# Kernel optimization log

Hardware: AMD Instinct MI355X
Metric: run time of the kernel (lower is better)

## Reference

```python
import jax, jax.numpy as jnp
import numpy as np

B, M, GRID = 4, 8192, 32          # batches, points per batch, voxel grid side
N = B * M
K = 8                              # knn neighbors (includes self at dist 0)
C_IN, C_OUT, H = 8, 8, 128
KEYB = 64                          # hash base (coords shifted +1 stay in [0,33])
EPS = 1e-5


def setup_inputs() -> dict:
    rng = np.random.default_rng(0)
    # unique occupied voxels per batch (ME SparseTensor requires unique coords)
    cs = []
    for b in range(B):
        lin = rng.choice(GRID ** 3, size=M, replace=False)
        x, y, z = lin // (GRID * GRID), (lin // GRID) % GRID, lin % GRID
        cs.append(np.stack([np.full(M, b), x, y, z], axis=1))
    coords = jnp.asarray(np.concatenate(cs, axis=0).astype(np.int32))  # [N,4]

    key = jax.random.key(0)
    ks = jax.random.split(key, 4)
    feats = jax.random.normal(ks[0], (N, C_IN), jnp.float32)
    w1 = jax.random.normal(ks[1], ((K + 1) * C_IN, H), jnp.float32) * 0.05  # 1x1 conv
    g1 = jnp.ones((H,), jnp.float32)
    b1 = jnp.zeros((H,), jnp.float32)
    w3 = jax.random.normal(ks[2], (27, H, H), jnp.float32) * 0.02          # 3^3 sparse conv
    g2 = jnp.ones((H,), jnp.float32)
    b2 = jnp.zeros((H,), jnp.float32)
    w_out = jax.random.normal(ks[3], (H, 2 * C_OUT), jnp.float32) * 0.05   # 1x1 conv
    return dict(coords=coords, feats=feats, w1=w1, g1=g1, b1=b1,
                w3=w3, g2=g2, b2=b2, w_out=w_out)


def _knn_idx(coords):
    # per-batch brute-force kNN on xyz (batch column segments the search)
    xyz = coords[:, 1:].astype(jnp.float32).reshape(B, M, 3)
    d2 = jnp.sum((xyz[:, :, None, :] - xyz[:, None, :, :]) ** 2, -1)  # [B,M,M]
    _, idx = jax.lax.top_k(-d2, K)                                     # [B,M,K]
    return (idx + (jnp.arange(B) * M)[:, None, None]).reshape(N, K)


def _bn(x, g, b):
    mu = jnp.mean(x, axis=0)
    var = jnp.var(x, axis=0)
    return (x - mu) * jax.lax.rsqrt(var + EPS) * g + b


def reference(coords, feats, w1, g1, b1, w3, g2, b2, w_out):
    # --- kNN gather-and-build: [center || k neighbor feats] -> (k+1)*C_in ---
    nbr = _knn_idx(coords)                                        # [N,K] int
    combined = jnp.concatenate([feats[:, None, :], feats[nbr]], axis=1)
    combined = combined.reshape(N, (K + 1) * C_IN)
    # --- neighbor_processor: 1x1 conv + BN + ReLU ---
    h = jax.nn.relu(_bn(combined @ w1, g1, b1))                   # [N,H]
    # --- context_predictor conv k=3: gather inputs at coord+offset via hash ---
    c = coords[:, 1:] + 1                                         # shift so offsets stay >= 0
    keys = ((coords[:, 0] * KEYB + c[:, 0]) * KEYB + c[:, 1]) * KEYB + c[:, 2]
    order = jnp.argsort(keys)
    skeys = keys[order]
    offs = jnp.stack(jnp.meshgrid(*([jnp.arange(-1, 2)] * 3), indexing='ij'),
                     axis=-1).reshape(27, 3)                      # {-1,0,1}^3
    okey = (offs[:, 0] * KEYB + offs[:, 1]) * KEYB + offs[:, 2]   # [27]
    q = keys[None, :] + okey[:, None]                             # [27,N]
    pos = jnp.clip(jnp.searchsorted(skeys, q), 0, N - 1)
    valid = skeys[pos] == q                                       # [27,N]
    j = order[pos]                                                # [27,N]
    gathered = jnp.where(valid[..., None], h[j], 0.0)             # [27,N,H]
    h2 = jnp.einsum('onc,ocd->nd', gathered, w3)                  # [N,H]
    h2 = jax.nn.relu(_bn(h2, g2, b2))
    # --- final 1x1 conv -> mean/scale ---
    return h2 @ w_out                                             # [N, 2*C_OUT]
```

## Files before the change

### kernel.cpp

```cpp
#include <hip/hip_runtime.h>
#include <hip/hip_bf16.h>

#define B_   4
#define M_   8192
#define N_   32768
#define H_   128
#define EPS_ 1e-5f
#define TBL  1048576
#define GUARD 8192

typedef short short8 __attribute__((ext_vector_type(8)));
typedef float f32x4  __attribute__((ext_vector_type(4)));

__global__ __launch_bounds__(256) void prep_pack_kernel(const int* __restrict__ coords,
                                                        int* __restrict__ table,
                                                        int* __restrict__ packed,
                                                        int* __restrict__ keyb,
                                                        const float* __restrict__ w3,
                                                        ushort* __restrict__ w3f,
                                                        float* __restrict__ gsum1,
                                                        float* __restrict__ gsum2,
                                                        int* __restrict__ flagcnt,
                                                        unsigned int* __restrict__ hbz) {
    int bid = blockIdx.x, tid = threadIdx.x;
    if (bid < 128) {
        int n = bid * 256 + tid;
        int b = coords[4*n+0], x = coords[4*n+1], y = coords[4*n+2], z = coords[4*n+3];
        packed[n] = (x << 10) | (y << 5) | z;
        int key = ((b*64 + x+1)*64 + y+1)*64 + (z+1);
        keyb[n] = key;
        table[key] = n;
        if (bid < 8)  gsum1[bid*256 + tid] = 0.f;
        if (bid == 0) gsum2[tid] = 0.f;
        if (bid == 8 && tid < 64) hbz[tid] = 0u;
        if (bid == 9 && tid == 0) *flagcnt = 0;
        return;
    }
    int t = (bid - 128) * 256 + tid;
    int lane = t & 63;
    int ct   = (t >> 6) & 7;
    int ks   = (t >> 9) & 3;
    int o    = t >> 11;
    int quad = lane >> 4, l15 = lane & 15;
    int n = ct*16 + l15;
    const float* src = w3 + o*16384;
    ushort out8[8];
#pragma unroll
    for (int j = 0; j < 8; ++j) {
        int c = ks*32 + quad*8 + j;
        float v = src[c*128 + n];
        __hip_bfloat16 bv = __float2bfloat16(v);
        ushort u; __builtin_memcpy(&u, &bv, 2);
        out8[j] = u;
    }
    *(uint4*)&w3f[t*8] = *(uint4*)out8;
}

__global__ __launch_bounds__(256) void knn_window_kernel(const int* __restrict__ table,
                                                         const int* __restrict__ keyb,
                                                         int* __restrict__ nbr,
                                                         int* __restrict__ flagcnt,
                                                         int* __restrict__ flaglist) {
    __shared__ int okey_sh[93], d2_sh[93];
    __shared__ int tops[256 * 8];
    __shared__ int ncnt;
    int tid = threadIdx.x;
    if (tid == 0) ncnt = 0;
    __syncthreads();
    if (tid < 125) {
        int dx = tid / 25 - 2, rr = tid % 25, dy = rr / 5 - 2, dz = rr % 5 - 2;
        int d2 = dx*dx + dy*dy + dz*dz;
        if (d2 <= 8) {
            int p = atomicAdd(&ncnt, 1);
            okey_sh[p] = dx * 4096 + dy * 64 + dz;
            d2_sh[p]   = d2;
        }
    }
    __syncthreads();

    int q   = blockIdx.x * 64 + (tid >> 2);
    int sub = tid & 3;
    int kb  = keyb[q];

    int top[8];
#pragma unroll
    for (int k = 0; k < 8; ++k) top[k] = 0x7FFFFFFF;

    int base = sub * 24;
    int cnt  = (sub == 3) ? 21 : 24;
    for (int i = 0; i < cnt; ++i) {
        int idx = base + i;
        int j = table[kb + okey_sh[idx]];
        if (j >= 0) {
            int key = (d2_sh[idx] << 13) | (j & 8191);
            if (key < top[7]) {
#pragma unroll
                for (int k = 7; k >= 1; --k)
                    top[k] = (key < top[k]) ? max(key, top[k-1]) : top[k];
                top[0] = min(key, top[0]);
            }
        }
    }
#pragma unroll
    for (int k = 0; k < 8; ++k) tops[tid*8 + k] = top[k];
    __syncthreads();

    if (sub == 0) {
        const int* L = &tops[tid*8];
        int ia0 = 0, ia1 = 0, ia2 = 0, ia3 = 0;
        int res[8];
#pragma unroll
        for (int k = 0; k < 8; ++k) {
            int v0 = L[ia0], v1 = L[8 + ia1], v2 = L[16 + ia2], v3 = L[24 + ia3];
            int m01 = min(v0, v1), m23 = min(v2, v3);
            int m = min(m01, m23);
            res[k] = m;
            if (m == v0) ++ia0; else if (m == v1) ++ia1;
            else if (m == v2) ++ia2; else ++ia3;
        }
        int bb = q & ~(M_-1);
        if ((res[7] >> 13) <= 8) {
#pragma unroll
            for (int k = 0; k < 8; ++k) nbr[q*8 + k] = bb + (res[k] & 8191);
        } else {
            int pos = atomicAdd(flagcnt, 1);
            flaglist[pos] = q;
        }
    }
}

__global__ __launch_bounds__(256) void knn_bf_kernel(const int* __restrict__ packed,
                                                     const int* __restrict__ flagcnt,
                                                     const int* __restrict__ flaglist,
                                                     int* __restrict__ nbr) {
    __shared__ int tops[256 * 8];
    int tid = threadIdx.x;
    int cnt = *flagcnt;
    for (int f = blockIdx.x; f < cnt; f += gridDim.x) {
        int n = flaglist[f];
        int bb = n & ~(M_-1);
        int p = packed[n];
        int qx = (p >> 10) & 31, qy = (p >> 5) & 31, qz = p & 31;
        int top[8];
#pragma unroll
        for (int k = 0; k < 8; ++k) top[k] = 0x7FFFFFFF;
        for (int j = tid; j < M_; j += 256) {
            int c = packed[bb + j];
            int dx = qx - ((c >> 10) & 31);
            int dy = qy - ((c >> 5) & 31);
            int dz = qz - (c & 31);
            int d2 = dx*dx + dy*dy + dz*dz;
            int key = (d2 << 13) | j;
            if (key < top[7]) {
#pragma unroll
                for (int k = 7; k >= 1; --k)
                    top[k] = (key < top[k]) ? max(key, top[k-1]) : top[k];
                top[0] = min(key, top[0]);
            }
        }
#pragma unroll
        for (int k = 0; k < 8; ++k) tops[tid*8 + k] = top[k];
        __syncthreads();
        for (int stride = 128; stride >= 1; stride >>= 1) {
            if (tid < stride) {
                int* A  = &tops[tid*8];
                int* Bp = &tops[(tid+stride)*8];
                int r[8]; int ia = 0, ib = 0;
#pragma unroll
                for (int k = 0; k < 8; ++k) {
                    int a = A[ia], b2 = Bp[ib];
                    if (a <= b2) { r[k] = a; ++ia; } else { r[k] = b2; ++ib; }
                }
#pragma unroll
                for (int k = 0; k < 8; ++k) A[k] = r[k];
            }
            __syncthreads();
        }
        if (tid == 0) {
#pragma unroll
            for (int k = 0; k < 8; ++k) nbr[n*8 + k] = bb + (tops[k] & 8191);
        }
        __syncthreads();
    }
}

__global__ __launch_bounds__(256) void h1_kernel(const float* __restrict__ feats,
                                                 const int* __restrict__ nbr,
                                                 const float* __restrict__ w1,
                                                 float* __restrict__ hpre,
                                                 float* __restrict__ gsum1) {
    __shared__ float comb[16][72];
    __shared__ float ssum[256], ssq[256];
    int tid = threadIdx.x;
    int rowbase = blockIdx.x * 16;
    if (tid < 144) {
        int r = tid / 9, s = tid % 9;
        int grow = rowbase + r;
        int idx = (s == 0) ? grow : nbr[grow*8 + (s-1)];
        const float4* f = (const float4*)(feats + idx * 8);
        float4 a = f[0], b = f[1];
        float* dp = &comb[r][s*8];
        dp[0]=a.x; dp[1]=a.y; dp[2]=a.z; dp[3]=a.w;
        dp[4]=b.x; dp[5]=b.y; dp[6]=b.z; dp[7]=b.w;
    }
    __syncthreads();
    int c = tid & 127, rh = tid >> 7;
    float acc[8];
#pragma unroll
    for (int i = 0; i < 8; ++i) acc[i] = 0.f;
    for (int s = 0; s < 72; ++s) {
        float w = w1[s*128 + c];
#pragma unroll
        for (int i = 0; i < 8; ++i)
            acc[i] += comb[rh*8 + i][s] * w;
    }
    float s = 0.f, q = 0.f;
#pragma unroll
    for (int i = 0; i < 8; ++i) {
        hpre[(rowbase + rh*8 + i)*128 + c] = acc[i];
        s += acc[i]; q += acc[i]*acc[i];
    }
    ssum[tid] = s; ssq[tid] = q;
    __syncthreads();
    if (tid < 128) {
        float S = ssum[tid] + ssum[tid+128];
        float Q = ssq[tid]  + ssq[tid+128];
        float* g = gsum1 + (blockIdx.x & 7) * 256;
        atomicAdd(&g[tid], S);
        atomicAdd(&g[128 + tid], Q);
    }
}

__global__ __launch_bounds__(256) void bnrelu_bf16_kernel(const float* __restrict__ x,
                                                          const float* __restrict__ gsum1,
                                                          const float* __restrict__ g1,
                                                          const float* __restrict__ b1,
                                                          ushort* __restrict__ y) {
    __shared__ float sc[128], sh[128];
    int tid = threadIdx.x;
    if (tid < 128) {
        float s = 0.f, q = 0.f;
#pragma unroll
        for (int r = 0; r < 8; ++r) {
            s += gsum1[r*256 + tid];
            q += gsum1[r*256 + 128 + tid];
        }
        float mu  = s / (float)N_;
        float var = q / (float)N_ - mu*mu;
        float inv = rsqrtf(var + EPS_);
        float scv = inv * g1[tid];
        sc[tid] = scv;
        sh[tid] = b1[tid] - mu * scv;
    }
    __syncthreads();
    int i = blockIdx.x * 256 + tid;
    float4 v = ((const float4*)x)[i];
    int c = (i * 4) & 127;
    v.x = fmaxf(0.f, v.x*sc[c]   + sh[c]);
    v.y = fmaxf(0.f, v.y*sc[c+1] + sh[c+1]);
    v.z = fmaxf(0.f, v.z*sc[c+2] + sh[c+2]);
    v.w = fmaxf(0.f, v.w*sc[c+3] + sh[c+3]);
    ushort o[4];
#pragma unroll
    for (int k = 0; k < 4; ++k) {
        float f = (&v.x)[k];
        __hip_bfloat16 bv = __float2bfloat16(f);
        __builtin_memcpy(&o[k], &bv, 2);
    }
    ((ushort4*)y)[i] = make_ushort4(o[0], o[1], o[2], o[3]);
}

#define CONV3_LDS 145408
__global__ __launch_bounds__(512) void conv3_mfma_kernel(const ushort* __restrict__ hb,
                                                         const ushort* __restrict__ w3f,
                                                         const int* __restrict__ table,
                                                         const int* __restrict__ keyb,
                                                         float* __restrict__ h2,
                                                         float* __restrict__ gsum) {
    extern __shared__ char smem_raw[];
    ushort* Asb = (ushort*)smem_raw;
    ushort* Bsb = (ushort*)(smem_raw + 65536);
    int*    jsh = (int*)(smem_raw + 131072);
    int*    kbsh= (int*)(smem_raw + 144896);

    int tid = threadIdx.x;
    int lane = tid & 63, wid = tid >> 6;
    int quad = lane >> 4, l15 = lane & 15;
    int bid = blockIdx.x;
    int swz = (bid & 7) * 32 + (bid >> 3);
    int rowbase = swz * 128;
    int wr = wid >> 1;
    int cb = (wid & 1) * 4;

    if (tid < 128) kbsh[tid] = keyb[rowbase + tid];
    __syncthreads();
    for (int t = tid; t < 27*128; t += 512) {
        int o = t >> 7, r = t & 127;
        int dx = o/9 - 1, dy = (o/3)%3 - 1, dz = o%3 - 1;
        jsh[t] = table[kbsh[r] + dx*4096 + dy*64 + dz];
    }
    __syncthreads();

#pragma unroll
    for (int i = 0; i < 4; ++i) {
        int flat = i*512 + tid;
        int r = flat >> 4, cp = flat & 15;
        int j = jsh[r];
        const ushort* asrc = hb + j*128 + ((cp ^ (r & 15)) << 3);
        __builtin_amdgcn_global_load_lds(
            (const __attribute__((address_space(1))) unsigned int*)asrc,
            (__attribute__((address_space(3))) unsigned int*)&Asb[flat << 3],
            16, 0, 0);
        __builtin_amdgcn_global_load_lds(
            (const __attribute__((address_space(1))) unsigned int*)(w3f + (flat << 3)),
            (__attribute__((address_space(3))) unsigned int*)&Bsb[flat << 3],
            16, 0, 0);
    }
    __syncthreads();

    f32x4 acc[2][4];
#pragma unroll
    for (int i = 0; i < 2; ++i)
#pragma unroll
        for (int c = 0; c < 4; ++c)
            acc[i][c] = (f32x4){0.f, 0.f, 0.f, 0.f};

    int cur = 0;
#pragma unroll 1
    for (int o = 0; o < 27; ++o) {
        if (o < 26) {
            int obase = (o + 1) << 7;
            const ushort* wsrc = w3f + ((o + 1) << 14);
            int dst = (cur ^ 1) * 16384;
#pragma unroll
            for (int i = 0; i < 4; ++i) {
                int flat = i*512 + tid;
                int r = flat >> 4, cp = flat & 15;
                int j = jsh[obase + r];
                const ushort* asrc = hb + j*128 + ((cp ^ (r & 15)) << 3);
                __builtin_amdgcn_global_load_lds(
                    (const __attribute__((address_space(1))) unsigned int*)asrc,
                    (__attribute__((address_space(3))) unsigned int*)&Asb[dst + (flat << 3)],
                    16, 0, 0);
                __builtin_amdgcn_global_load_lds(
                    (const __attribute__((address_space(1))) unsigned int*)(wsrc + (flat << 3)),
                    (__attribute__((address_space(3))) unsigned int*)&Bsb[dst + (flat << 3)],
                    16, 0, 0);
            }
        }
        const ushort* Ac = Asb + cur*16384;
        const ushort* Bc = Bsb + cur*16384;
#pragma unroll
        for (int ks = 0; ks < 4; ++ks) {
            short8 af[2], bfr[4];
#pragma unroll
            for (int i = 0; i < 2; ++i) {
                int lr = wr*32 + i*16 + l15;
                int chunk = (ks*4 + quad) ^ l15;
                af[i] = *(const short8*)&Ac[lr*128 + chunk*8];
            }
#pragma unroll
            for (int c = 0; c < 4; ++c)
                bfr[c] = *(const short8*)&Bc[((ks*8 + cb + c)*64 + lane) << 3];
#pragma unroll
            for (int i = 0; i < 2; ++i)
#pragma unroll
                for (int c = 0; c < 4; ++c)
                    acc[i][c] = __builtin_amdgcn_mfma_f32_16x16x32_bf16(af[i], bfr[c], acc[i][c], 0, 0, 0);
        }
        __syncthreads();
        cur ^= 1;
    }

    float s[4], q[4];
#pragma unroll
    for (int c = 0; c < 4; ++c) { s[c] = 0.f; q[c] = 0.f; }
#pragma unroll
    for (int i = 0; i < 2; ++i)
#pragma unroll
        for (int c = 0; c < 4; ++c)
#pragma unroll
            for (int r = 0; r < 4; ++r) {
                int row = rowbase + wr*32 + i*16 + quad*4 + r;
                int col = (cb + c)*16 + l15;
                float v = acc[i][c][r];
                h2[row*128 + col] = v;
                s[c] += v; q[c] += v*v;
            }
    float* red = (float*)smem_raw;
    if (tid < 256) red[tid] = 0.f;
    __syncthreads();
#pragma unroll
    for (int c = 0; c < 4; ++c) {
        int col = (cb + c)*16 + l15;
        atomicAdd(&red[col], s[c]);
        atomicAdd(&red[128 + col], q[c]);
    }
    __syncthreads();
    if (tid < 256) atomicAdd(&gsum[tid], red[tid]);
}

__global__ __launch_bounds__(256) void out_kernel(const float* __restrict__ h2,
                                                  const float* __restrict__ wout,
                                                  const float* __restrict__ gsum2,
                                                  const float* __restrict__ g2,
                                                  const float* __restrict__ b2,
                                                  float* __restrict__ out) {
    __shared__ float hrow[128][129];
    __shared__ float wsh[2048];
    __shared__ float sc[128], sh[128];
    int tid = threadIdx.x;
    if (tid < 128) {
        float s = gsum2[tid], q = gsum2[128 + tid];
        float mu  = s / (float)N_;
        float var = q / (float)N_ - mu*mu;
        float inv = rsqrtf(var + EPS_);
        float scv = inv * g2[tid];
        sc[tid] = scv;
        sh[tid] = b2[tid] - mu * scv;
    }
#pragma unroll
    for (int i = 0; i < 8; ++i) wsh[i*256 + tid] = wout[i*256 + tid];
    __syncthreads();

    int rowbase = blockIdx.x * 128;
#pragma unroll
    for (int i = 0; i < 16; ++i) {
        int flat = i*256 + tid;
        int row = flat >> 5, c4 = (flat & 31) * 4;
        float4 v = *(const float4*)&h2[(rowbase + row)*128 + c4];
        float4 scv = *(const float4*)&sc[c4];
        float4 shv = *(const float4*)&sh[c4];
        hrow[row][c4+0] = fmaxf(0.f, fmaf(v.x, scv.x, shv.x));
        hrow[row][c4+1] = fmaxf(0.f, fmaf(v.y, scv.y, shv.y));
        hrow[row][c4+2] = fmaxf(0.f, fmaf(v.z, scv.z, shv.z));
        hrow[row][c4+3] = fmaxf(0.f, fmaf(v.w, scv.w, shv.w));
    }
    __syncthreads();

    int row = tid >> 1, dbase = (tid & 1) * 8;
    float acc[8];
#pragma unroll
    for (int k = 0; k < 8; ++k) acc[k] = 0.f;
    for (int c = 0; c < 128; ++c) {
        float hv = hrow[row][c];
        float4 w0 = *(const float4*)&wsh[c*16 + dbase];
        float4 w1 = *(const float4*)&wsh[c*16 + dbase + 4];
        acc[0] = fmaf(hv, w0.x, acc[0]);
        acc[1] = fmaf(hv, w0.y, acc[1]);
        acc[2] = fmaf(hv, w0.z, acc[2]);
        acc[3] = fmaf(hv, w0.w, acc[3]);
        acc[4] = fmaf(hv, w1.x, acc[4]);
        acc[5] = fmaf(hv, w1.y, acc[5]);
        acc[6] = fmaf(hv, w1.z, acc[6]);
        acc[7] = fmaf(hv, w1.w, acc[7]);
    }
    float* op = out + (rowbase + row)*16 + dbase;
    *(float4*)op       = (float4){acc[0], acc[1], acc[2], acc[3]};
    *(float4*)(op + 4) = (float4){acc[4], acc[5], acc[6], acc[7]};
}

extern "C" void kernel_launch(void* const* d_in, const int* in_sizes, int n_in,
                              void* d_out, int out_size, void* d_ws, size_t ws_size,
                              hipStream_t stream) {
    const int*   coords = (const int*)d_in[0];
    const float* feats  = (const float*)d_in[1];
    const float* w1     = (const float*)d_in[2];
    const float* g1     = (const float*)d_in[3];
    const float* b1     = (const float*)d_in[4];
    const float* w3     = (const float*)d_in[5];
    const float* g2     = (const float*)d_in[6];
    const float* b2     = (const float*)d_in[7];
    const float* wout   = (const float*)d_in[8];
    float* out = (float*)d_out;

    char* ws = (char*)d_ws;
    int*    table_base = (int*)(ws);
    int*    table   = table_base + GUARD;
    int*    packed  = (int*)(ws + (4352u<<10));
    int*    keyb    = (int*)(ws + (4608u<<10));
    int*    nbr     = (int*)(ws + (4864u<<10));
    int*    flagcnt = (int*)(ws + (5888u<<10));
    int*    flaglist= (int*)(ws + (5892u<<10));
    float*  gsum2   = (float*)(ws + (6416u<<10));
    float*  gsum1   = (float*)(ws + (6420u<<10));
    ushort* w3f     = (ushort*)(ws + (6656u<<10));
    ushort* hb      = (ushort*)(ws + (7680u<<10));
    float*  h       = (float*)(ws + (15872u<<10));
    float*  h2      = h;

    static bool conv3_attr_set = false;
    if (!conv3_attr_set) {
        hipFuncSetAttribute(reinterpret_cast<const void*>(&conv3_mfma_kernel),
                            hipFuncAttributeMaxDynamicSharedMemorySize, CONV3_LDS);
        conv3_attr_set = true;
    }

    hipMemsetAsync(table_base, 0xFF, (TBL + GUARD) * sizeof(int), stream);
    prep_pack_kernel <<<344, 256, 0, stream>>>(coords, table, packed, keyb, w3, w3f,
                                               gsum1, gsum2, flagcnt,
                                               (unsigned int*)(hb - 128));
    knn_window_kernel<<<N_/64, 256, 0, stream>>>(table, keyb, nbr, flagcnt, flaglist);
    knn_bf_kernel    <<<256, 256, 0, stream>>>(packed, flagcnt, flaglist, nbr);
    h1_kernel        <<<N_/16, 256, 0, stream>>>(feats, nbr, w1, h, gsum1);
    bnrelu_bf16_kernel<<<(N_*H_/4)/256, 256, 0, stream>>>(h, gsum1, g1, b1, hb);
    conv3_mfma_kernel<<<N_/128, 512, CONV3_LDS, stream>>>(hb, w3f, table, keyb, h2, gsum2);
    out_kernel       <<<N_/128, 256, 0, stream>>>(h2, wout, gsum2, g2, b2, out);
}
```

Before: 194.3 us.

## Fuse all pipeline stages into one cooperative persistent kernel with grid syncs

Replaces the memset and seven separate kernel launches with a single cooperative kernel of 256 blocks x 512 threads that runs every stage (table init, packing, kNN window and brute force, h1, BN/ReLU, MFMA conv, output) and separates them with grid.sync(). The aim is to remove launch overhead and inter-kernel gaps. In exchange, each stage runs at one block per CU with a fixed grid, so occupancy drops for stages that used many small blocks before. Grid-wide barriers also cost time, and the table memset now runs as a strided store loop.

Result: slower. 535.0 us (+175.3%).

```diff
diff --git a/kernel.cpp b/kernel.cpp
--- a/kernel.cpp
+++ b/kernel.cpp
@@ -1,5 +1,8 @@
 #include <hip/hip_runtime.h>
+#include <hip/hip_cooperative_groups.h>
 #include <hip/hip_bf16.h>
+
+namespace cg = cooperative_groups;
 
 #define B_   4
 #define M_   8192
@@ -8,456 +11,430 @@
 #define EPS_ 1e-5f
 #define TBL  1048576
 #define GUARD 8192
+#define NTHREADS 131072
 
 typedef short short8 __attribute__((ext_vector_type(8)));
 typedef float f32x4  __attribute__((ext_vector_type(4)));
 
-__global__ __launch_bounds__(256) void prep_pack_kernel(const int* __restrict__ coords,
-                                                        int* __restrict__ table,
-                                                        int* __restrict__ packed,
-                                                        int* __restrict__ keyb,
-                                                        const float* __restrict__ w3,
-                                                        ushort* __restrict__ w3f,
-                                                        float* __restrict__ gsum1,
-                                                        float* __restrict__ gsum2,
-                                                        int* __restrict__ flagcnt,
-                                                        unsigned int* __restrict__ hbz) {
-    int bid = blockIdx.x, tid = threadIdx.x;
-    if (bid < 128) {
-        int n = bid * 256 + tid;
+#define MEGA_LDS 145408
+
+__device__ __forceinline__ ushort f2bf(float f) {
+    __hip_bfloat16 bv = __float2bfloat16(f);
+    ushort u; __builtin_memcpy(&u, &bv, 2);
+    return u;
+}
+
+__global__ __launch_bounds__(512, 1) void mega_kernel(
+        const int* __restrict__ coords, const float* __restrict__ feats,
+        const float* __restrict__ w1, const float* __restrict__ g1,
+        const float* __restrict__ b1, const float* __restrict__ w3,
+        const float* __restrict__ g2, const float* __restrict__ b2,
+        const float* __restrict__ wout, float* __restrict__ out,
+        int* __restrict__ table_base, int* __restrict__ packed,
+        int* __restrict__ keyb, int* __restrict__ nbr,
+        int* __restrict__ flagcnt, int* __restrict__ flaglist,
+        float* __restrict__ gsum1, float* __restrict__ gsum2,
+        ushort* __restrict__ w3f, ushort* __restrict__ hb,
+        float* __restrict__ h) {
+    extern __shared__ char smem_raw[];
+    cg::grid_group grid = cg::this_grid();
+    int tid = threadIdx.x, bid = blockIdx.x;
+    int gid = bid * 512 + tid;
+    int* table = table_base + GUARD;
+    float* h2 = h;
+
+    for (int idx = gid; idx < TBL + GUARD; idx += NTHREADS) table_base[idx] = -1;
+    if (gid < N_) {
+        int n = gid;
         int b = coords[4*n+0], x = coords[4*n+1], y = coords[4*n+2], z = coords[4*n+3];
         packed[n] = (x << 10) | (y << 5) | z;
-        int key = ((b*64 + x+1)*64 + y+1)*64 + (z+1);
-        keyb[n] = key;
-        table[key] = n;
-        if (bid < 8)  gsum1[bid*256 + tid] = 0.f;
-        if (bid == 0) gsum2[tid] = 0.f;
-        if (bid == 8 && tid < 64) hbz[tid] = 0u;
-        if (bid == 9 && tid == 0) *flagcnt = 0;
-        return;
-    }
-    int t = (bid - 128) * 256 + tid;
-    int lane = t & 63;
-    int ct   = (t >> 6) & 7;
-    int ks   = (t >> 9) & 3;
-    int o    = t >> 11;
-    int quad = lane >> 4, l15 = lane & 15;
-    int n = ct*16 + l15;
-    const float* src = w3 + o*16384;
-    ushort out8[8];
-#pragma unroll
-    for (int j = 0; j < 8; ++j) {
-        int c = ks*32 + quad*8 + j;
-        float v = src[c*128 + n];
-        __hip_bfloat16 bv = __float2bfloat16(v);
-        ushort u; __builtin_memcpy(&u, &bv, 2);
-        out8[j] = u;
-    }
-    *(uint4*)&w3f[t*8] = *(uint4*)out8;
-}
-
-__global__ __launch_bounds__(256) void knn_window_kernel(const int* __restrict__ table,
-                                                         const int* __restrict__ keyb,
-                                                         int* __restrict__ nbr,
-                                                         int* __restrict__ flagcnt,
-                                                         int* __restrict__ flaglist) {
-    __shared__ int okey_sh[93], d2_sh[93];
-    __shared__ int tops[256 * 8];
-    __shared__ int ncnt;
-    int tid = threadIdx.x;
-    if (tid == 0) ncnt = 0;
-    __syncthreads();
-    if (tid < 125) {
-        int dx = tid / 25 - 2, rr = tid % 25, dy = rr / 5 - 2, dz = rr % 5 - 2;
-        int d2 = dx*dx + dy*dy + dz*dz;
-        if (d2 <= 8) {
-            int p = atomicAdd(&ncnt, 1);
-            okey_sh[p] = dx * 4096 + dy * 64 + dz;
-            d2_sh[p]   = d2;
-        }
-    }
-    __syncthreads();
-
-    int q   = blockIdx.x * 64 + (tid >> 2);
-    int sub = tid & 3;
-    int kb  = keyb[q];
-
-    int top[8];
-#pragma unroll
-    for (int k = 0; k < 8; ++k) top[k] = 0x7FFFFFFF;
-
-    int base = sub * 24;
-    int cnt  = (sub == 3) ? 21 : 24;
-    for (int i = 0; i < cnt; ++i) {
-        int idx = base + i;
-        int j = table[kb + okey_sh[idx]];
-        if (j >= 0) {
-            int key = (d2_sh[idx] << 13) | (j & 8191);
-            if (key < top[7]) {
-#pragma unroll
-                for (int k = 7; k >= 1; --k)
-                    top[k] = (key < top[k]) ? max(key, top[k-1]) : top[k];
-                top[0] = min(key, top[0]);
-            }
-        }
-    }
-#pragma unroll
-    for (int k = 0; k < 8; ++k) tops[tid*8 + k] = top[k];
-    __syncthreads();
-
-    if (sub == 0) {
-        const int* L = &tops[tid*8];
-        int ia0 = 0, ia1 = 0, ia2 = 0, ia3 = 0;
-        int res[8];
-#pragma unroll
-        for (int k = 0; k < 8; ++k) {
-            int v0 = L[ia0], v1 = L[8 + ia1], v2 = L[16 + ia2], v3 = L[24 + ia3];
-            int m01 = min(v0, v1), m23 = min(v2, v3);
-            int m = min(m01, m23);
-            res[k] = m;
-            if (m == v0) ++ia0; else if (m == v1) ++ia1;
-            else if (m == v2) ++ia2; else ++ia3;
-        }
-        int bb = q & ~(M_-1);
-        if ((res[7] >> 13) <= 8) {
-#pragma unroll
-            for (int k = 0; k < 8; ++k) nbr[q*8 + k] = bb + (res[k] & 8191);
-        } else {
-            int pos = atomicAdd(flagcnt, 1);
-            flaglist[pos] = q;
-        }
-    }
-}
-
-__global__ __launch_bounds__(256) void knn_bf_kernel(const int* __restrict__ packed,
-                                                     const int* __restrict__ flagcnt,
-                                                     const int* __restrict__ flaglist,
-                                                     int* __restrict__ nbr) {
-    __shared__ int tops[256 * 8];
-    int tid = threadIdx.x;
-    int cnt = *flagcnt;
-    for (int f = blockIdx.x; f < cnt; f += gridDim.x) {
-        int n = flaglist[f];
-        int bb = n & ~(M_-1);
-        int p = packed[n];
-        int qx = (p >> 10) & 31, qy = (p >> 5) & 31, qz = p & 31;
+        keyb[n] = ((b*64 + x+1)*64 + y+1)*64 + (z+1);
+    }
+    if (gid < 55296) {
+        int t = gid;
+        int tl = t & 63;
+        int ct = (t >> 6) & 7, ks = (t >> 9) & 3, o = t >> 11;
+        int tq = tl >> 4, t15 = tl & 15;
+        int n = ct*16 + t15;
+        const float* src = w3 + o*16384;
+        ushort out8[8];
+#pragma unroll
+        for (int j = 0; j < 8; ++j)
+            out8[j] = f2bf(src[(ks*32 + tq*8 + j)*128 + n]);
+        *(uint4*)&w3f[t*8] = *(uint4*)out8;
+    }
+    if (gid < 2048) gsum1[gid] = 0.f;
+    if (gid < 256)  gsum2[gid] = 0.f;
+    if (gid < 64)   ((unsigned int*)(hb - 128))[gid] = 0u;
+    if (gid == 0)   *flagcnt = 0;
+    grid.sync();
+
+    if (gid < N_) table[keyb[gid]] = gid;
+    grid.sync();
+
+    {
+        int* okey_sh = (int*)smem_raw;
+        int* d2_sh   = (int*)(smem_raw + 512);
+        int* tops    = (int*)(smem_raw + 1024);
+        __shared__ int ncnt;
+        if (tid == 0) ncnt = 0;
+        __syncthreads();
+        if (tid < 125) {
+            int dx = tid / 25 - 2, rr = tid % 25, dy = rr / 5 - 2, dz = rr % 5 - 2;
+            int d2 = dx*dx + dy*dy + dz*dz;
+            if (d2 <= 8) {
+                int p = atomicAdd(&ncnt, 1);
+                okey_sh[p] = dx * 4096 + dy * 64 + dz;
+                d2_sh[p]   = d2;
+            }
+        }
+        __syncthreads();
+
+        int q   = bid * 128 + (tid >> 2);
+        int sub = tid & 3;
+        int kb  = keyb[q];
         int top[8];
 #pragma unroll
         for (int k = 0; k < 8; ++k) top[k] = 0x7FFFFFFF;
-        for (int j = tid; j < M_; j += 256) {
-            int c = packed[bb + j];
-            int dx = qx - ((c >> 10) & 31);
-            int dy = qy - ((c >> 5) & 31);
-            int dz = qz - (c & 31);
-            int d2 = dx*dx + dy*dy + dz*dz;
-            int key = (d2 << 13) | j;
-            if (key < top[7]) {
-#pragma unroll
-                for (int k = 7; k >= 1; --k)
-                    top[k] = (key < top[k]) ? max(key, top[k-1]) : top[k];
-                top[0] = min(key, top[0]);
+        int base = sub * 24;
+        int cnt  = (sub == 3) ? 21 : 24;
+        for (int i = 0; i < cnt; ++i) {
+            int idx = base + i;
+            int j = table[kb + okey_sh[idx]];
+            if (j >= 0) {
+                int key = (d2_sh[idx] << 13) | (j & 8191);
+                if (key < top[7]) {
+#pragma unroll
+                    for (int k = 7; k >= 1; --k)
+                        top[k] = (key < top[k]) ? max(key, top[k-1]) : top[k];
+                    top[0] = min(key, top[0]);
+                }
             }
         }
 #pragma unroll
         for (int k = 0; k < 8; ++k) tops[tid*8 + k] = top[k];
         __syncthreads();
-        for (int stride = 128; stride >= 1; stride >>= 1) {
-            if (tid < stride) {
-                int* A  = &tops[tid*8];
-                int* Bp = &tops[(tid+stride)*8];
-                int r[8]; int ia = 0, ib = 0;
-#pragma unroll
-                for (int k = 0; k < 8; ++k) {
-                    int a = A[ia], b2 = Bp[ib];
-                    if (a <= b2) { r[k] = a; ++ia; } else { r[k] = b2; ++ib; }
-                }
-#pragma unroll
-                for (int k = 0; k < 8; ++k) A[k] = r[k];
-            }
+
+        if (sub == 0) {
+            const int* L = &tops[tid*8];
+            int ia0 = 0, ia1 = 0, ia2 = 0, ia3 = 0;
+            int res[8];
+#pragma unroll
+            for (int k = 0; k < 8; ++k) {
+                int v0 = L[ia0], v1 = L[8 + ia1], v2 = L[16 + ia2], v3 = L[24 + ia3];
+                int m01 = min(v0, v1), m23 = min(v2, v3);
+                int m = min(m01, m23);
+                res[k] = m;
+                if (m == v0) ++ia0; else if (m == v1) ++ia1;
+                else if (m == v2) ++ia2; else ++ia3;
+            }
+            int bb = q & ~(M_-1);
+            if ((res[7] >> 13) <= 8) {
+#pragma unroll
+                for (int k = 0; k < 8; ++k) nbr[q*8 + k] = bb + (res[k] & 8191);
+            } else {
+                int pos = atomicAdd(flagcnt, 1);
+                flaglist[pos] = q;
+            }
+        }
+    }
+    grid.sync();
+
+    {
+        int* tops = (int*)smem_raw;
+        int cnt = atomicAdd(flagcnt, 0);
+        for (int f = bid; f < cnt; f += 256) {
+            int n = flaglist[f];
+            int bb = n & ~(M_-1);
+            int p = packed[n];
+            int qx = (p >> 10) & 31, qy = (p >> 5) & 31, qz = p & 31;
+            int top[8];
+#pragma unroll
+            for (int k = 0; k < 8; ++k) top[k] = 0x7FFFFFFF;
+            for (int j = tid; j < M_; j += 512) {
+                int c = packed[bb + j];
+                int dx = qx - ((c >> 10) & 31);
+                int dy = qy - ((c >> 5) & 31);
+                int dz = qz - (c & 31);
+                int d2 = dx*dx + dy*dy + dz*dz;
+                int key = (d2 << 13) | j;
+                if (key < top[7]) {
+#pragma unroll
+                    for (int k = 7; k >= 1; --k)
+                        top[k] = (key < top[k]) ? max(key, top[k-1]) : top[k];
+                    top[0] = min(key, top[0]);
+                }
+            }
+#pragma unroll
+            for (int k = 0; k < 8; ++k) tops[tid*8 + k] = top[k];
             __syncthreads();
-        }
-        if (tid == 0) {
-#pragma unroll
-            for (int k = 0; k < 8; ++k) nbr[n*8 + k] = bb + (tops[k] & 8191);
-        }
-        __syncthreads();
-    }
-}
-
-__global__ __launch_bounds__(256) void h1_kernel(const float* __restrict__ feats,
-                                                 const int* __restrict__ nbr,
-                                                 const float* __restrict__ w1,
-                                                 float* __restrict__ hpre,
-                                                 float* __restrict__ gsum1) {
-    __shared__ float comb[16][72];
-    __shared__ float ssum[256], ssq[256];
-    int tid = threadIdx.x;
-    int rowbase = blockIdx.x * 16;
-    if (tid < 144) {
-        int r = tid / 9, s = tid % 9;
-        int grow = rowbase + r;
-        int idx = (s == 0) ? grow : nbr[grow*8 + (s-1)];
-        const float4* f = (const float4*)(feats + idx * 8);
-        float4 a = f[0], b = f[1];
-        float* dp = &comb[r][s*8];
-        dp[0]=a.x; dp[1]=a.y; dp[2]=a.z; dp[3]=a.w;
-        dp[4]=b.x; dp[5]=b.y; dp[6]=b.z; dp[7]=b.w;
-    }
-    __syncthreads();
-    int c = tid & 127, rh = tid >> 7;
-    float acc[8];
-#pragma unroll
-    for (int i = 0; i < 8; ++i) acc[i] = 0.f;
-    for (int s = 0; s < 72; ++s) {
-        float w = w1[s*128 + c];
-#pragma unroll
-        for (int i = 0; i < 8; ++i)
-            acc[i] += comb[rh*8 + i][s] * w;
-    }
-    float s = 0.f, q = 0.f;
-#pragma unroll
-    for (int i = 0; i < 8; ++i) {
-        hpre[(rowbase + rh*8 + i)*128 + c] = acc[i];
-        s += acc[i]; q += acc[i]*acc[i];
-    }
-    ssum[tid] = s; ssq[tid] = q;
-    __syncthreads();
-    if (tid < 128) {
-        float S = ssum[tid] + ssum[tid+128];
-        float Q = ssq[tid]  + ssq[tid+128];
-        float* g = gsum1 + (blockIdx.x & 7) * 256;
-        atomicAdd(&g[tid], S);
-        atomicAdd(&g[128 + tid], Q);
-    }
-}
-
-__global__ __launch_bounds__(256) void bnrelu_bf16_kernel(const float* __restrict__ x,
-                                                          const float* __restrict__ gsum1,
-                                                          const float* __restrict__ g1,
-                                                          const float* __restrict__ b1,
-                                                          ushort* __restrict__ y) {
-    __shared__ float sc[128], sh[128];
-    int tid = threadIdx.x;
-    if (tid < 128) {
-        float s = 0.f, q = 0.f;
-#pragma unroll
-        for (int r = 0; r < 8; ++r) {
-            s += gsum1[r*256 + tid];
-            q += gsum1[r*256 + 128 + tid];
-        }
-        float mu  = s / (float)N_;
-        float var = q / (float)N_ - mu*mu;
-        float inv = rsqrtf(var + EPS_);
-        float scv = inv * g1[tid];
-        sc[tid] = scv;
-        sh[tid] = b1[tid] - mu * scv;
-    }
-    __syncthreads();
-    int i = blockIdx.x * 256 + tid;
-    float4 v = ((const float4*)x)[i];
-    int c = (i * 4) & 127;
-    v.x = fmaxf(0.f, v.x*sc[c]   + sh[c]);
-    v.y = fmaxf(0.f, v.y*sc[c+1] + sh[c+1]);
-    v.z = fmaxf(0.f, v.z*sc[c+2] + sh[c+2]);
-    v.w = fmaxf(0.f, v.w*sc[c+3] + sh[c+3]);
-    ushort o[4];
-#pragma unroll
-    for (int k = 0; k < 4; ++k) {
-        float f = (&v.x)[k];
-        __hip_bfloat16 bv = __float2bfloat16(f);
-        __builtin_memcpy(&o[k], &bv, 2);
-    }
-    ((ushort4*)y)[i] = make_ushort4(o[0], o[1], o[2], o[3]);
-}
-
-#define CONV3_LDS 145408
-__global__ __launch_bounds__(512) void conv3_mfma_kernel(const ushort* __restrict__ hb,
-                                                         const ushort* __restrict__ w3f,
-                                                         const int* __restrict__ table,
-                                                         const int* __restrict__ keyb,
-                                                         float* __restrict__ h2,
-                                                         float* __restrict__ gsum) {
-    extern __shared__ char smem_raw[];
-    ushort* Asb = (ushort*)smem_raw;
-    ushort* Bsb = (ushort*)(smem_raw + 65536);
-    int*    jsh = (int*)(smem_raw + 131072);
-    int*    kbsh= (int*)(smem_raw + 144896);
-
-    int tid = threadIdx.x;
-    int lane = tid & 63, wid = tid >> 6;
-    int quad = lane >> 4, l15 = lane & 15;
-    int bid = blockIdx.x;
-    int swz = (bid & 7) * 32 + (bid >> 3);
-    int rowbase = swz * 128;
-    int wr = wid >> 1;
-    int cb = (wid & 1) * 4;
-
-    if (tid < 128) kbsh[tid] = keyb[rowbase + tid];
-    __syncthreads();
-    for (int t = tid; t < 27*128; t += 512) {
-        int o = t >> 7, r = t & 127;
-        int dx = o/9 - 1, dy = (o/3)%3 - 1, dz = o%3 - 1;
-        jsh[t] = table[kbsh[r] + dx*4096 + dy*64 + dz];
-    }
-    __syncthreads();
-
-#pragma unroll
-    for (int i = 0; i < 4; ++i) {
-        int flat = i*512 + tid;
-        int r = flat >> 4, cp = flat & 15;
-        int j = jsh[r];
-        const ushort* asrc = hb + j*128 + ((cp ^ (r & 15)) << 3);
-        __builtin_amdgcn_global_load_lds(
-            (const __attribute__((address_space(1))) unsigned int*)asrc,
-            (__attribute__((address_space(3))) unsigned int*)&Asb[flat << 3],
-            16, 0, 0);
-        __builtin_amdgcn_global_load_lds(
-            (const __attribute__((address_space(1))) unsigned int*)(w3f + (flat << 3)),
-            (__attribute__((address_space(3))) unsigned int*)&Bsb[flat << 3],
-            16, 0, 0);
-    }
-    __syncthreads();
-
-    f32x4 acc[2][4];
-#pragma unroll
-    for (int i = 0; i < 2; ++i)
-#pragma unroll
-        for (int c = 0; c < 4; ++c)
-            acc[i][c] = (f32x4){0.f, 0.f, 0.f, 0.f};
-
-    int cur = 0;
+            for (int stride = 256; stride >= 1; stride >>= 1) {
+                if (tid < stride) {
+                    int* A  = &tops[tid*8];
+                    int* Bp = &tops[(tid+stride)*8];
+                    int r[8]; int ia = 0, ib = 0;
+#pragma unroll
+                    for (int k = 0; k < 8; ++k) {
+                        int a = A[ia], b2v = Bp[ib];
+                        if (a <= b2v) { r[k] = a; ++ia; } else { r[k] = b2v; ++ib; }
+                    }
+#pragma unroll
+                    for (int k = 0; k < 8; ++k) A[k] = r[k];
+                }
+                __syncthreads();
+            }
+            if (tid == 0) {
+#pragma unroll
+                for (int k = 0; k < 8; ++k) nbr[n*8 + k] = bb + (tops[k] & 8191);
+            }
+            __syncthreads();
+        }
+    }
+    grid.sync();
+
+    {
+        float (*comb)[72] = (float(*)[72])smem_raw;
+        float* ssum = (float*)(smem_raw + 12288);
+        float* ssq  = (float*)(smem_raw + 14336);
+        int c = tid & 127, rh = tid >> 7;
+        float sAcc = 0.f, qAcc = 0.f;
+        for (int it = 0; it < 4; ++it) {
+            int rowbase = bid*128 + it*32;
+            __syncthreads();
+            if (tid < 288) {
+                int r = tid / 9, s = tid % 9;
+                int grow = rowbase + r;
+                int idx = (s == 0) ? grow : nbr[grow*8 + (s-1)];
+                const float4* f4 = (const float4*)(feats + idx * 8);
+                float4 a = f4[0], b4 = f4[1];
+                float* dp = &comb[r][s*8];
+                dp[0]=a.x; dp[1]=a.y; dp[2]=a.z; dp[3]=a.w;
+                dp[4]=b4.x; dp[5]=b4.y; dp[6]=b4.z; dp[7]=b4.w;
+            }
+            __syncthreads();
+            float acc[8];
+#pragma unroll
+            for (int i = 0; i < 8; ++i) acc[i] = 0.f;
+            for (int s = 0; s < 72; ++s) {
+                float w = w1[s*128 + c];
+#pragma unroll
+                for (int i = 0; i < 8; ++i)
+                    acc[i] += comb[rh*8 + i][s] * w;
+            }
+#pragma unroll
+            for (int i = 0; i < 8; ++i) {
+                h[(rowbase + rh*8 + i)*128 + c] = acc[i];
+                sAcc += acc[i]; qAcc += acc[i]*acc[i];
+            }
+        }
+        ssum[tid] = sAcc; ssq[tid] = qAcc;
+        __syncthreads();
+        if (tid < 128) {
+            float S = ssum[tid] + ssum[tid+128] + ssum[tid+256] + ssum[tid+384];
+            float Q = ssq[tid]  + ssq[tid+128]  + ssq[tid+256]  + ssq[tid+384];
+            float* g = gsum1 + (bid & 7) * 256;
+            atomicAdd(&g[tid], S);
+            atomicAdd(&g[128 + tid], Q);
+        }
+    }
+    grid.sync();
+
+    {
+        float* sc = (float*)smem_raw;
+        float* sh = (float*)(smem_raw + 512);
+        if (tid < 128) {
+            float s = 0.f, q = 0.f;
+#pragma unroll
+            for (int r = 0; r < 8; ++r) {
+                s += gsum1[r*256 + tid];
+                q += gsum1[r*256 + 128 + tid];
+            }
+            float mu  = s / (float)N_;
+            float var = q / (float)N_ - mu*mu;
+            float inv = rsqrtf(var + EPS_);
+            float scv = inv * g1[tid];
+            sc[tid] = scv;
+            sh[tid] = b1[tid] - mu * scv;
+        }
+        __syncthreads();
+        for (int i = gid; i < N_*H_/4; i += NTHREADS) {
+            float4 v = ((const float4*)h)[i];
+            int c = (i * 4) & 127;
+            v.x = fmaxf(0.f, v.x*sc[c]   + sh[c]);
+            v.y = fmaxf(0.f, v.y*sc[c+1] + sh[c+1]);
+            v.z = fmaxf(0.f, v.z*sc[c+2] + sh[c+2]);
+            v.w = fmaxf(0.f, v.w*sc[c+3] + sh[c+3]);
+            ((ushort4*)hb)[i] = make_ushort4(f2bf(v.x), f2bf(v.y), f2bf(v.z), f2bf(v.w));
+        }
+    }
+    grid.sync();
+
+    {
+        ushort* Asb = (ushort*)smem_raw;
+        ushort* Bsb = (ushort*)(smem_raw + 65536);
+        int*    jsh = (int*)(smem_raw + 131072);
+        int*    kbsh= (int*)(smem_raw + 144896);
+        int lane = tid & 63, wid = tid >> 6;
+        int quad = lane >> 4, l15 = lane & 15;
+        int swz = (bid & 7) * 32 + (bid >> 3);
+        int rowbase = swz * 128;
+        int wr = wid >> 1;
+        int cb = (wid & 1) * 4;
+
+        if (tid < 128) kbsh[tid] = keyb[rowbase + tid];
+        __syncthreads();
+        for (int t = tid; t < 27*128; t += 512) {
+            int o = t >> 7, r = t & 127;
+            int dx = o/9 - 1, dy = (o/3)%3 - 1, dz = o%3 - 1;
+            jsh[t] = table[kbsh[r] + dx*4096 + dy*64 + dz];
+        }
+        __syncthreads();
+
+#pragma unroll
+        for (int i = 0; i < 4; ++i) {
+            int flat = i*512 + tid;
+            int r = flat >> 4, cp = flat & 15;
+            int j = jsh[r];
+            const ushort* asrc = hb + j*128 + ((cp ^ (r & 15)) << 3);
+            __builtin_amdgcn_global_load_lds(
+                (const __attribute__((address_space(1))) unsigned int*)asrc,
+                (__attribute__((address_space(3))) unsigned int*)&Asb[flat << 3],
+                16, 0, 0);
+            __builtin_amdgcn_global_load_lds(
+                (const __attribute__((address_space(1))) unsigned int*)(w3f + (flat << 3)),
+                (__attribute__((address_space(3))) unsigned int*)&Bsb[flat << 3],
+                16, 0, 0);
+        }
+        __syncthreads();
+
+        f32x4 acc[2][4];
+#pragma unroll
+        for (int i = 0; i < 2; ++i)
+#pragma unroll
+            for (int c = 0; c < 4; ++c)
+                acc[i][c] = (f32x4){0.f, 0.f, 0.f, 0.f};
+
+        int cur = 0;
 #pragma unroll 1
-    for (int o = 0; o < 27; ++o) {
-        if (o < 26) {
-            int obase = (o + 1) << 7;
-            const ushort* wsrc = w3f + ((o + 1) << 14);
-            int dst = (cur ^ 1) * 16384;
-#pragma unroll
-            for (int i = 0; i < 4; ++i) {
-                int flat = i*512 + tid;
-                int r = flat >> 4, cp = flat & 15;
-                int j = jsh[obase + r];
-                const ushort* asrc = hb + j*128 + ((cp ^ (r & 15)) << 3);
-                __builtin_amdgcn_global_load_lds(
-                    (const __attribute__((address_space(1))) unsigned int*)asrc,
-                    (__attribute__((address_space(3))) unsigned int*)&Asb[dst + (flat << 3)],
-                    16, 0, 0);
-                __builtin_amdgcn_global_load_lds(
-                    (const __attribute__((address_space(1))) unsigned int*)(wsrc + (flat << 3)),
-                    (__attribute__((address_space(3))) unsigned int*)&Bsb[dst + (flat << 3)],
-                    16, 0, 0);
-            }
-        }
-        const ushort* Ac = Asb + cur*16384;
-        const ushort* Bc = Bsb + cur*16384;
-#pragma unroll
-        for (int ks = 0; ks < 4; ++ks) {
-            short8 af[2], bfr[4];
-#pragma unroll
-            for (int i = 0; i < 2; ++i) {
-                int lr = wr*32 + i*16 + l15;
-                int chunk = (ks*4 + quad) ^ l15;
-                af[i] = *(const short8*)&Ac[lr*128 + chunk*8];
-            }
+        for (int o = 0; o < 27; ++o) {
+            if (o < 26) {
+                int obase = (o + 1) << 7;
+                const ushort* wsrc = w3f + ((o + 1) << 14);
+                int dst = (cur ^ 1) * 16384;
+#pragma unroll
+                for (int i = 0; i < 4; ++i) {
+                    int flat = i*512 + tid;
+                    int r = flat >> 4, cp = flat & 15;
+                    int j = jsh[obase + r];
+                    const ushort* asrc = hb + j*128 + ((cp ^ (r & 15)) << 3);
+                    __builtin_amdgcn_global_load_lds(
+                        (const __attribute__((address_space(1))) unsigned int*)asrc,
+                        (__attribute__((address_space(3))) unsigned int*)&Asb[dst + (flat << 3)],
+                        16, 0, 0);
+                    __builtin_amdgcn_global_load_lds(
+                        (const __attribute__((address_space(1))) unsigned int*)(wsrc + (flat << 3)),
+                        (__attribute__((address_space(3))) unsigned int*)&Bsb[dst + (flat << 3)],
+                        16, 0, 0);
+                }
+            }
+            const ushort* Ac = Asb + cur*16384;
+            const ushort* Bc = Bsb + cur*16384;
+#pragma unroll
+            for (int ks = 0; ks < 4; ++ks) {
+                short8 af[2], bfr[4];
+#pragma unroll
+                for (int i = 0; i < 2; ++i) {
+                    int lr = wr*32 + i*16 + l15;
+                    int chunk = (ks*4 + quad) ^ l15;
+                    af[i] = *(const short8*)&Ac[lr*128 + chunk*8];
+                }
+#pragma unroll
+                for (int c = 0; c < 4; ++c)
+                    bfr[c] = *(const short8*)&Bc[((ks*8 + cb + c)*64 + lane) << 3];
+#pragma unroll
+                for (int i = 0; i < 2; ++i)
+#pragma unroll
+                    for (int c = 0; c < 4; ++c)
+                        acc[i][c] = __builtin_amdgcn_mfma_f32_16x16x32_bf16(af[i], bfr[c], acc[i][c], 0, 0, 0);
+            }
+            __syncthreads();
+            cur ^= 1;
+        }
+
+        float s[4], q[4];
+#pragma unroll
+        for (int c = 0; c < 4; ++c) { s[c] = 0.f; q[c] = 0.f; }
+#pragma unroll
+        for (int i = 0; i < 2; ++i)
 #pragma unroll
             for (int c = 0; c < 4; ++c)
-                bfr[c] = *(const short8*)&Bc[((ks*8 + cb + c)*64 + lane) << 3];
-#pragma unroll
-            for (int i = 0; i < 2; ++i)
-#pragma unroll
-                for (int c = 0; c < 4; ++c)
-                    acc[i][c] = __builtin_amdgcn_mfma_f32_16x16x32_bf16(af[i], bfr[c], acc[i][c], 0, 0, 0);
-        }
-        __syncthreads();
-        cur ^= 1;
-    }
-
-    float s[4], q[4];
-#pragma unroll
-    for (int c = 0; c < 4; ++c) { s[c] = 0.f; q[c] = 0.f; }
-#pragma unroll
-    for (int i = 0; i < 2; ++i)
-#pragma unroll
-        for (int c = 0; c < 4; ++c)
-#pragma unroll
-            for (int r = 0; r < 4; ++r) {
-                int row = rowbase + wr*32 + i*16 + quad*4 + r;
-                int col = (cb + c)*16 + l15;
-                float v = acc[i][c][r];
-                h2[row*128 + col] = v;
-                s[c] += v; q[c] += v*v;
-            }
-    float* red = (float*)smem_raw;
-    if (tid < 256) red[tid] = 0.f;
-    __syncthreads();
-#pragma unroll
-    for (int c = 0; c < 4; ++c) {
-        int col = (cb + c)*16 + l15;
-        atomicAdd(&red[col], s[c]);
-        atomicAdd(&red[128 + col], q[c]);
-    }
-    __syncthreads();
-    if (tid < 256) atomicAdd(&gsum[tid], red[tid]);
-}
-
-__global__ __launch_bounds__(256) void out_kernel(const float* __restrict__ h2,
-                                                  const float* __restrict__ wout,
-                                                  const float* __restrict__ gsum2,
-                                                  const float* __restrict__ g2,
-                                                  const float* __restrict__ b2,
-                                                  float* __restrict__ out) {
-    __shared__ float hrow[128][129];
-    __shared__ float wsh[2048];
-    __shared__ float sc[128], sh[128];
-    int tid = threadIdx.x;
-    if (tid < 128) {
-        float s = gsum2[tid], q = gsum2[128 + tid];
-        float mu  = s / (float)N_;
-        float var = q / (float)N_ - mu*mu;
-        float inv = rsqrtf(var + EPS_);
-        float scv = inv * g2[tid];
-        sc[tid] = scv;
-        sh[tid] = b2[tid] - mu * scv;
-    }
-#pragma unroll
-    for (int i = 0; i < 8; ++i) wsh[i*256 + tid] = wout[i*256 + tid];
-    __syncthreads();
-
-    int rowbase = blockIdx.x * 128;
-#pragma unroll
-    for (int i = 0; i < 16; ++i) {
-        int flat = i*256 + tid;
-        int row = flat >> 5, c4 = (flat & 31) * 4;
-        float4 v = *(const float4*)&h2[(rowbase + row)*128 + c4];
-        float4 scv = *(const float4*)&sc[c4];
-        float4 shv = *(const float4*)&sh[c4];
-        hrow[row][c4+0] = fmaxf(0.f, fmaf(v.x, scv.x, shv.x));
-        hrow[row][c4+1] = fmaxf(0.f, fmaf(v.y, scv.y, shv.y));
-        hrow[row][c4+2] = fmaxf(0.f, fmaf(v.z, scv.z, shv.z));
-        hrow[row][c4+3] = fmaxf(0.f, fmaf(v.w, scv.w, shv.w));
-    }
-    __syncthreads();
-
-    int row = tid >> 1, dbase = (tid & 1) * 8;
-    float acc[8];
-#pragma unroll
-    for (int k = 0; k < 8; ++k) acc[k] = 0.f;
-    for (int c = 0; c < 128; ++c) {
-        float hv = hrow[row][c];
-        float4 w0 = *(const float4*)&wsh[c*16 + dbase];
-        float4 w1 = *(const float4*)&wsh[c*16 + dbase + 4];
-        acc[0] = fmaf(hv, w0.x, acc[0]);
-        acc[1] = fmaf(hv, w0.y, acc[1]);
-        acc[2] = fmaf(hv, w0.z, acc[2]);
-        acc[3] = fmaf(hv, w0.w, acc[3]);
-        acc[4] = fmaf(hv, w1.x, acc[4]);
-        acc[5] = fmaf(hv, w1.y, acc[5]);
-        acc[6] = fmaf(hv, w1.z, acc[6]);
-        acc[7] = fmaf(hv, w1.w, acc[7]);
-    }
-    float* op = out + (rowbase + row)*16 + dbase;
-    *(float4*)op       = (float4){acc[0], acc[1], acc[2], acc[3]};
-    *(float4*)(op + 4) = (float4){acc[4], acc[5], acc[6], acc[7]};
+#pragma unroll
+                for (int r = 0; r < 4; ++r) {
+                    int row = rowbase + wr*32 + i*16 + quad*4 + r;
+                    int col = (cb + c)*16 + l15;
+                    float v = acc[i][c][r];
+                    h2[row*128 + col] = v;
+                    s[c] += v; q[c] += v*v;
+                }
+        float* red = (float*)smem_raw;
+        __syncthreads();
+        if (tid < 256) red[tid] = 0.f;
+        __syncthreads();
+#pragma unroll
+        for (int c = 0; c < 4; ++c) {
+            int col = (cb + c)*16 + l15;
+            atomicAdd(&red[col], s[c]);
+            atomicAdd(&red[128 + col], q[c]);
+        }
+        __syncthreads();
+        if (tid < 256) atomicAdd(&gsum2[tid], red[tid]);
+    }
+    grid.sync();
+
+    {
+        float (*hrow)[129] = (float(*)[129])smem_raw;
+        float* wsh = (float*)(smem_raw + 66048);
+        float* sc  = (float*)(smem_raw + 74240);
+        float* sh  = (float*)(smem_raw + 74752);
+        if (tid < 128) {
+            float s = gsum2[tid], q = gsum2[128 + tid];
+            float mu  = s / (float)N_;
+            float var = q / (float)N_ - mu*mu;
+            float inv = rsqrtf(var + EPS_);
+            float scv = inv * g2[tid];
+            sc[tid] = scv;
+            sh[tid] = b2[tid] - mu * scv;
+        }
+        for (int i = tid; i < 2048; i += 512) wsh[i] = wout[i];
+        __syncthreads();
+
+        int rowbase = bid * 128;
+#pragma unroll
+        for (int i = 0; i < 8; ++i) {
+            int flat = i*512 + tid;
+            int row = flat >> 5, c4 = (flat & 31) * 4;
+            float4 v = *(const float4*)&h2[(rowbase + row)*128 + c4];
+            float4 scv = *(const float4*)&sc[c4];
+            float4 shv = *(const float4*)&sh[c4];
+            hrow[row][c4+0] = fmaxf(0.f, fmaf(v.x, scv.x, shv.x));
+            hrow[row][c4+1] = fmaxf(0.f, fmaf(v.y, scv.y, shv.y));
+            hrow[row][c4+2] = fmaxf(0.f, fmaf(v.z, scv.z, shv.z));
+            hrow[row][c4+3] = fmaxf(0.f, fmaf(v.w, scv.w, shv.w));
+        }
+        __syncthreads();
+
+        int row = tid >> 2, dbase = (tid & 3) * 4;
+        float a0 = 0.f, a1 = 0.f, a2 = 0.f, a3 = 0.f;
+        for (int c = 0; c < 128; ++c) {
+            float hv = hrow[row][c];
+            float4 w = *(const float4*)&wsh[c*16 + dbase];
+            a0 = fmaf(hv, w.x, a0);
+            a1 = fmaf(hv, w.y, a1);
+            a2 = fmaf(hv, w.z, a2);
+            a3 = fmaf(hv, w.w, a3);
+        }
+        *(float4*)&out[(rowbase + row)*16 + dbase] = (float4){a0, a1, a2, a3};
+    }
 }
 
 extern "C" void kernel_launch(void* const* d_in, const int* in_sizes, int n_in,
@@ -476,7 +453,6 @@
 
     char* ws = (char*)d_ws;
     int*    table_base = (int*)(ws);
-    int*    table   = table_base + GUARD;
     int*    packed  = (int*)(ws + (4352u<<10));
     int*    keyb    = (int*)(ws + (4608u<<10));
     int*    nbr     = (int*)(ws + (4864u<<10));
@@ -487,23 +463,21 @@
     ushort* w3f     = (ushort*)(ws + (6656u<<10));
     ushort* hb      = (ushort*)(ws + (7680u<<10));
     float*  h       = (float*)(ws + (15872u<<10));
-    float*  h2      = h;
-
-    static bool conv3_attr_set = false;
-    if (!conv3_attr_set) {
-        hipFuncSetAttribute(reinterpret_cast<const void*>(&conv3_mfma_kernel),
-                            hipFuncAttributeMaxDynamicSharedMemorySize, CONV3_LDS);
-        conv3_attr_set = true;
-    }
-
-    hipMemsetAsync(table_base, 0xFF, (TBL + GUARD) * sizeof(int), stream);
-    prep_pack_kernel <<<344, 256, 0, stream>>>(coords, table, packed, keyb, w3, w3f,
-                                               gsum1, gsum2, flagcnt,
-                                               (unsigned int*)(hb - 128));
-    knn_window_kernel<<<N_/64, 256, 0, stream>>>(table, keyb, nbr, flagcnt, flaglist);
-    knn_bf_kernel    <<<256, 256, 0, stream>>>(packed, flagcnt, flaglist, nbr);
-    h1_kernel        <<<N_/16, 256, 0, stream>>>(feats, nbr, w1, h, gsum1);
-    bnrelu_bf16_kernel<<<(N_*H_/4)/256, 256, 0, stream>>>(h, gsum1, g1, b1, hb);
-    conv3_mfma_kernel<<<N_/128, 512, CONV3_LDS, stream>>>(hb, w3f, table, keyb, h2, gsum2);
-    out_kernel       <<<N_/128, 256, 0, stream>>>(h2, wout, gsum2, g2, b2, out);
+
+    static bool attr_set = false;
+    if (!attr_set) {
+        hipFuncSetAttribute(reinterpret_cast<const void*>(&mega_kernel),
+                            hipFuncAttributeMaxDynamicSharedMemorySize, MEGA_LDS);
+        attr_set = true;
+    }
+
+    void* kargs[] = {
+        (void*)&coords, (void*)&feats, (void*)&w1, (void*)&g1, (void*)&b1,
+        (void*)&w3, (void*)&g2, (void*)&b2, (void*)&wout, (void*)&out,
+        (void*)&table_base, (void*)&packed, (void*)&keyb, (void*)&nbr,
+        (void*)&flagcnt, (void*)&flaglist, (void*)&gsum1, (void*)&gsum2,
+        (void*)&w3f, (void*)&hb, (void*)&h
+    };
+    hipLaunchCooperativeKernel(reinterpret_cast<const void*>(&mega_kernel),
+                               dim3(256), dim3(512), kargs, MEGA_LDS, stream);
 }
```
